# Kernel optimization log

Measured on AMD Instinct MI355X. Metric: run time of the kernel, lower is better.

The kernel has to match this reference:

```python
import jax, jax.numpy as jnp
import numpy as np

SPARSITY = 0.8  # fraction of weights zeroed (random unstructured mask)

def setup_inputs() -> dict:
    key = jax.random.key(0)
    k1, k2, k3, k4 = jax.random.split(key, 4)
    B, S, D_IN, D_OUT = 4, 2048, 4096, 4096
    x = jax.random.normal(k1, (B, S, D_IN), dtype=jnp.float32)
    weight = jax.random.normal(k2, (D_OUT, D_IN), dtype=jnp.float32) * 0.02
    bias = jax.random.normal(k3, (D_OUT,), dtype=jnp.float32) * 0.02
    # fixed binary mask: keep with prob (1 - sparsity)
    mask = (jax.random.uniform(k4, (D_OUT, D_IN)) >= SPARSITY).astype(jnp.float32)
    return {"x": x, "weight": weight, "bias": bias, "mask": mask}

def reference(x, weight, bias, mask):
    # w = weight * mask; y = x @ w.T + b   (F.linear semantics)
    w = weight * mask                      # [O, I]
    y = jnp.einsum('bsi,oi->bso', x, w)    # [B, S, O]
    return y + bias
```

## Files before the change

### kernel.cpp

```cpp
#include <hip/hip_runtime.h>
#include <hip/hip_bf16.h>
#include <stdint.h>

#define M_DIM 8192
#define N_DIM 4096
#define K_DIM 4096

#define BM 256
#define BN 256
#define BK 64
#define NT (K_DIM / BK)

typedef __attribute__((ext_vector_type(8))) __bf16 bf16x8;
typedef __attribute__((ext_vector_type(4))) float floatx4;

__device__ inline unsigned f2b(float f) {
    union { float f; unsigned u; } v; v.f = f;
    return (v.u + 0x7FFFu + ((v.u >> 16) & 1u)) >> 16;
}
__device__ inline unsigned pk2(float lo, float hi) {
    return (f2b(lo) & 0xFFFFu) | (f2b(hi) << 16);
}

__device__ inline void async_load16(const void* g, void* l) {
    __builtin_amdgcn_global_load_lds(
        (const __attribute__((address_space(1))) unsigned int*)(unsigned long long)g,
        (__attribute__((address_space(3))) unsigned int*)(unsigned int)(unsigned long long)l,
        16, 0, 0);
}

#define SFENCE() asm volatile("" ::: "memory")

#define CVT_GRID 2048
#define CVT_XBLK 1120
__global__ __launch_bounds__(256)
void cvt_all(const float4* __restrict__ x, const float4* __restrict__ w,
             const float4* __restrict__ m, uint4* __restrict__ xb,
             uint4* __restrict__ wb, int nx8, int nw8) {
    if ((int)blockIdx.x < CVT_XBLK) {
        int i = blockIdx.x * 256 + threadIdx.x;
        const int stride = CVT_XBLK * 256;
        for (; i < nx8; i += stride) {
            float4 a = x[2 * i], b = x[2 * i + 1];
            uint4 o;
            o.x = pk2(a.x, a.y); o.y = pk2(a.z, a.w);
            o.z = pk2(b.x, b.y); o.w = pk2(b.z, b.w);
            xb[i] = o;
        }
    } else {
        int i = ((int)blockIdx.x - CVT_XBLK) * 256 + threadIdx.x;
        const int stride = (CVT_GRID - CVT_XBLK) * 256;
        for (; i < nw8; i += stride) {
            float4 w0 = w[2 * i], w1 = w[2 * i + 1];
            float4 m0 = m[2 * i], m1 = m[2 * i + 1];
            uint4 o;
            o.x = pk2(w0.x * m0.x, w0.y * m0.y);
            o.y = pk2(w0.z * m0.z, w0.w * m0.w);
            o.z = pk2(w1.x * m1.x, w1.y * m1.y);
            o.w = pk2(w1.z * m1.z, w1.w * m1.w);
            wb[i] = o;
        }
    }
}

__global__ __launch_bounds__(512, 2)
void gemm_8phase(const __hip_bfloat16* __restrict__ A,
                 const __hip_bfloat16* __restrict__ B,
                 const float* __restrict__ bias,
                 float* __restrict__ C) {
    __shared__ __hip_bfloat16 As[2][2][128][64];
    __shared__ __hip_bfloat16 Bs[2][2][128][64];

    const int t    = threadIdx.x;
    const int lane = t & 63;
    const int wave = t >> 6;
    const int wm   = wave >> 2;
    const int wn   = wave & 3;
    const int lm   = lane & 15;
    const int h4   = lane >> 4;

    const int wg = (blockIdx.x & 7) * 64 + (blockIdx.x >> 3);
    const int m0 = (wg >> 4) * BM;
    const int n0 = (wg & 15) * BN;

    const int srow = t >> 3;
    const int schk = t & 7;
    const int sx   = schk ^ (srow & 7);

    const __hip_bfloat16* gA[2][2];
    const __hip_bfloat16* gB[2][2];
#pragma unroll
    for (int h = 0; h < 2; h++)
#pragma unroll
        for (int r = 0; r < 2; r++) {
            gA[h][r] = A + (size_t)(m0 + h * 128 + r * 64 + srow) * K_DIM + sx * 8;
            gB[h][r] = B + (size_t)(n0 + h * 128 + r * 64 + srow) * K_DIM + sx * 8;
        }

#define STAGE_A(b, h, r, tt) \
    async_load16(gA[h][r] + (size_t)(tt) * BK, &As[b][h][(r) * 64 + srow][schk * 8])
#define STAGE_B(b, h, r, tt) \
    async_load16(gB[h][r] + (size_t)(tt) * BK, &Bs[b][h][(r) * 64 + srow][schk * 8])

    const int cs0 = ((h4)     ^ (lm & 7)) * 8;
    const int cs1 = ((4 + h4) ^ (lm & 7)) * 8;

#define LDA(b, i, kk) \
    (*(const bf16x8*)&As[b][wm][(i) * 16 + lm][(kk) ? cs1 : cs0])
#define LDB(b, j, kk) \
    (*(const bf16x8*)&Bs[b][wn >> 1][(wn & 1) * 64 + (j) * 16 + lm][(kk) ? cs1 : cs0])

    floatx4 acc[8][4] = {};
    bf16x8 af[4][2], b01[2][2], b23[2][2];

#define MFMA16(bi, bj, B_)                                                    \
    __builtin_amdgcn_s_setprio(1);                                            \
    _Pragma("unroll") for (int i = 0; i < 4; i++)                             \
    _Pragma("unroll") for (int j = 0; j < 2; j++)                             \
    _Pragma("unroll") for (int kk = 0; kk < 2; kk++)                          \
        acc[(bi) + i][(bj) + j] = __builtin_amdgcn_mfma_f32_16x16x32_bf16(    \
            af[i][kk], B_[j][kk], acc[(bi) + i][(bj) + j], 0, 0, 0);          \
    __builtin_amdgcn_s_setprio(0);

#define KTILE(b, nb, ss)                                                      \
  { const int s_ = (ss);                                                      \
                                               \
    _Pragma("unroll") for (int i = 0; i < 4; i++) {                           \
        af[i][0] = LDA(b, i, 0); af[i][1] = LDA(b, i, 1); }                   \
    _Pragma("unroll") for (int j = 0; j < 2; j++) {                           \
        b01[j][0] = LDB(b, j, 0); b01[j][1] = LDB(b, j, 1); }                 \
    if (s_ + 1 < NT) { STAGE_A(nb, 0, 1, s_ + 1); STAGE_A(nb, 1, 1, s_ + 1); }\
    asm volatile("s_waitcnt lgkmcnt(8)" ::: "memory");                        \
    SFENCE(); __builtin_amdgcn_s_barrier();                                   \
    asm volatile("s_waitcnt lgkmcnt(0)" ::: "memory");                        \
    MFMA16(0, 0, b01)                                                         \
    SFENCE(); __builtin_amdgcn_s_barrier(); SFENCE();                         \
                                               \
    _Pragma("unroll") for (int j = 0; j < 2; j++) {                           \
        b23[j][0] = LDB(b, 2 + j, 0); b23[j][1] = LDB(b, 2 + j, 1); }         \
    if (s_ + 2 < NT) { STAGE_A(b, 0, 0, s_ + 2); STAGE_A(b, 1, 0, s_ + 2); }  \
    SFENCE(); __builtin_amdgcn_s_barrier();                                   \
    asm volatile("s_waitcnt lgkmcnt(0)" ::: "memory");                        \
    MFMA16(0, 2, b23)                                                         \
    SFENCE(); __builtin_amdgcn_s_barrier(); SFENCE();                         \
                                               \
    _Pragma("unroll") for (int i = 0; i < 4; i++) {                           \
        af[i][0] = LDA(b, 4 + i, 0); af[i][1] = LDA(b, 4 + i, 1); }           \
    if (s_ + 2 < NT) { STAGE_B(b, 0, 0, s_ + 2); STAGE_B(b, 0, 1, s_ + 2); }  \
    SFENCE(); __builtin_amdgcn_s_barrier();                                   \
    asm volatile("s_waitcnt lgkmcnt(0)" ::: "memory");                        \
    MFMA16(4, 0, b01)                                                         \
    SFENCE(); __builtin_amdgcn_s_barrier(); SFENCE();                         \
                                               \
    if (s_ + 2 < NT) { STAGE_B(b, 1, 0, s_ + 2); STAGE_B(b, 1, 1, s_ + 2); }  \
    MFMA16(4, 2, b23)                                                         \
    if (s_ + 2 < NT) asm volatile("s_waitcnt vmcnt(6)" ::: "memory");         \
    else             asm volatile("s_waitcnt vmcnt(0)" ::: "memory");         \
    SFENCE(); __builtin_amdgcn_s_barrier(); SFENCE();                         \
  }

    STAGE_A(0, 0, 0, 0); STAGE_A(0, 1, 0, 0);
    STAGE_A(0, 0, 1, 0); STAGE_A(0, 1, 1, 0);
    STAGE_B(0, 0, 0, 0); STAGE_B(0, 0, 1, 0);
    STAGE_B(0, 1, 0, 0); STAGE_B(0, 1, 1, 0);
    STAGE_A(1, 0, 0, 1); STAGE_A(1, 1, 0, 1);
    STAGE_B(1, 0, 0, 1); STAGE_B(1, 0, 1, 1);
    STAGE_B(1, 1, 0, 1); STAGE_B(1, 1, 1, 1);
    asm volatile("s_waitcnt vmcnt(6)" ::: "memory");
    __builtin_amdgcn_s_barrier();
    SFENCE();

    for (int s = 0; s < NT; s += 2) {
        KTILE(0, 1, s)
        KTILE(1, 0, s + 1)
    }

    float bv[4];
#pragma unroll
    for (int j = 0; j < 4; j++)
        bv[j] = bias[n0 + wn * 64 + j * 16 + lm];
    const int row_base = m0 + wm * 128 + h4 * 4;
    const int col_base = n0 + wn * 64 + lm;
#pragma unroll
    for (int i = 0; i < 8; i++)
#pragma unroll
        for (int j = 0; j < 4; j++) {
            const int col = col_base + j * 16;
#pragma unroll
            for (int r = 0; r < 4; r++)
                C[(size_t)(row_base + i * 16 + r) * N_DIM + col] =
                    acc[i][j][r] + bv[j];
        }
}

extern "C" void kernel_launch(void* const* d_in, const int* in_sizes, int n_in,
                              void* d_out, int out_size, void* d_ws, size_t ws_size,
                              hipStream_t stream) {
    const float* x    = (const float*)d_in[0];
    const float* w    = (const float*)d_in[1];
    const float* bias = (const float*)d_in[2];
    const float* mask = (const float*)d_in[3];
    float* out = (float*)d_out;

    __hip_bfloat16* xb = (__hip_bfloat16*)d_ws;
    __hip_bfloat16* wb = xb + (size_t)M_DIM * K_DIM;

    cvt_all<<<dim3(CVT_GRID), dim3(256), 0, stream>>>(
        (const float4*)x, (const float4*)w, (const float4*)mask,
        (uint4*)xb, (uint4*)wb, M_DIM * K_DIM / 8, N_DIM * K_DIM / 8);
    gemm_8phase<<<dim3(512), dim3(512), 0, stream>>>(xb, wb, bias, out);
}
```

Before: 527.2 us.

## Double-buffer A fragments and prefetch next tile's LDS reads across K-tiles

Splits the A-fragment registers into two sets (rows 0-3 and 4-7), so the LDS reads for the next K-tile's first phase can be issued at the end of the current tile. This lets each MFMA phase rely on barriers alone, without explicit lgkmcnt waits. Global-to-LDS staging is reordered, and the tail branches are replaced by re-staging the current tile into the same buffer. The aim is to overlap LDS reads with MFMA work and cut stall points, at the cost of more live registers and some redundant global loads on the last tiles.

```diff
diff --git a/kernel.cpp b/kernel.cpp
--- a/kernel.cpp
+++ b/kernel.cpp
@@ -111,69 +111,75 @@
     (*(const bf16x8*)&Bs[b][wn >> 1][(wn & 1) * 64 + (j) * 16 + lm][(kk) ? cs1 : cs0])
 
     floatx4 acc[8][4] = {};
-    bf16x8 af[4][2], b01[2][2], b23[2][2];
-
-#define MFMA16(bi, bj, B_)                                                    \
+    bf16x8 af03[4][2], af47[4][2], b01[2][2], b23[2][2];
+
+#define MFMA16(bi, bj, A_, B_)                                                \
     __builtin_amdgcn_s_setprio(1);                                            \
     _Pragma("unroll") for (int i = 0; i < 4; i++)                             \
     _Pragma("unroll") for (int j = 0; j < 2; j++)                             \
     _Pragma("unroll") for (int kk = 0; kk < 2; kk++)                          \
         acc[(bi) + i][(bj) + j] = __builtin_amdgcn_mfma_f32_16x16x32_bf16(    \
-            af[i][kk], B_[j][kk], acc[(bi) + i][(bj) + j], 0, 0, 0);          \
+            A_[i][kk], B_[j][kk], acc[(bi) + i][(bj) + j], 0, 0, 0);          \
     __builtin_amdgcn_s_setprio(0);
 
 #define KTILE(b, nb, ss)                                                      \
   { const int s_ = (ss);                                                      \
-                                               \
-    _Pragma("unroll") for (int i = 0; i < 4; i++) {                           \
-        af[i][0] = LDA(b, i, 0); af[i][1] = LDA(b, i, 1); }                   \
-    _Pragma("unroll") for (int j = 0; j < 2; j++) {                           \
-        b01[j][0] = LDB(b, j, 0); b01[j][1] = LDB(b, j, 1); }                 \
-    if (s_ + 1 < NT) { STAGE_A(nb, 0, 1, s_ + 1); STAGE_A(nb, 1, 1, s_ + 1); }\
-    asm volatile("s_waitcnt lgkmcnt(8)" ::: "memory");                        \
-    SFENCE(); __builtin_amdgcn_s_barrier();                                   \
-    asm volatile("s_waitcnt lgkmcnt(0)" ::: "memory");                        \
-    MFMA16(0, 0, b01)                                                         \
-    SFENCE(); __builtin_amdgcn_s_barrier(); SFENCE();                         \
-                                               \
+    const int tt = (s_ + 2 < NT) ? s_ + 2 : s_;   \
+                               \
     _Pragma("unroll") for (int j = 0; j < 2; j++) {                           \
         b23[j][0] = LDB(b, 2 + j, 0); b23[j][1] = LDB(b, 2 + j, 1); }         \
-    if (s_ + 2 < NT) { STAGE_A(b, 0, 0, s_ + 2); STAGE_A(b, 1, 0, s_ + 2); }  \
-    SFENCE(); __builtin_amdgcn_s_barrier();                                   \
-    asm volatile("s_waitcnt lgkmcnt(0)" ::: "memory");                        \
-    MFMA16(0, 2, b23)                                                         \
-    SFENCE(); __builtin_amdgcn_s_barrier(); SFENCE();                         \
-                                               \
+    SFENCE(); __builtin_amdgcn_s_barrier();                                   \
+    MFMA16(0, 0, af03, b01)                                                   \
+    SFENCE(); __builtin_amdgcn_s_barrier();                                   \
+            \
     _Pragma("unroll") for (int i = 0; i < 4; i++) {                           \
-        af[i][0] = LDA(b, 4 + i, 0); af[i][1] = LDA(b, 4 + i, 1); }           \
-    if (s_ + 2 < NT) { STAGE_B(b, 0, 0, s_ + 2); STAGE_B(b, 0, 1, s_ + 2); }  \
-    SFENCE(); __builtin_amdgcn_s_barrier();                                   \
-    asm volatile("s_waitcnt lgkmcnt(0)" ::: "memory");                        \
-    MFMA16(4, 0, b01)                                                         \
-    SFENCE(); __builtin_amdgcn_s_barrier(); SFENCE();                         \
-                                               \
-    if (s_ + 2 < NT) { STAGE_B(b, 1, 0, s_ + 2); STAGE_B(b, 1, 1, s_ + 2); }  \
-    MFMA16(4, 2, b23)                                                         \
-    if (s_ + 2 < NT) asm volatile("s_waitcnt vmcnt(6)" ::: "memory");         \
-    else             asm volatile("s_waitcnt vmcnt(0)" ::: "memory");         \
-    SFENCE(); __builtin_amdgcn_s_barrier(); SFENCE();                         \
+        af47[i][0] = LDA(b, 4 + i, 0); af47[i][1] = LDA(b, 4 + i, 1); }       \
+    STAGE_A(b, 0, 0, tt); STAGE_A(b, 1, 0, tt);                               \
+    SFENCE(); __builtin_amdgcn_s_barrier();                                   \
+    MFMA16(0, 2, af03, b23)                                                   \
+    SFENCE(); __builtin_amdgcn_s_barrier();                                   \
+                             \
+    STAGE_B(b, 0, 0, tt); STAGE_B(b, 0, 1, tt);                               \
+    STAGE_B(b, 1, 0, tt); STAGE_B(b, 1, 1, tt);                               \
+    SFENCE(); __builtin_amdgcn_s_barrier();                                   \
+    MFMA16(4, 0, af47, b01)                                                   \
+    SFENCE(); __builtin_amdgcn_s_barrier();                                   \
+    \
+    asm volatile("s_waitcnt vmcnt(6)" ::: "memory");                          \
+    if (s_ + 1 < NT) {                                                        \
+        _Pragma("unroll") for (int i = 0; i < 4; i++) {                       \
+            af03[i][0] = LDA(nb, i, 0); af03[i][1] = LDA(nb, i, 1); }         \
+        _Pragma("unroll") for (int j = 0; j < 2; j++) {                       \
+            b01[j][0] = LDB(nb, j, 0); b01[j][1] = LDB(nb, j, 1); }           \
+    }                                                                         \
+    STAGE_A(b, 0, 1, tt); STAGE_A(b, 1, 1, tt);                               \
+    SFENCE(); __builtin_amdgcn_s_barrier();                                   \
+    MFMA16(4, 2, af47, b23)                                                   \
+    SFENCE(); __builtin_amdgcn_s_barrier();                                   \
   }
 
     STAGE_A(0, 0, 0, 0); STAGE_A(0, 1, 0, 0);
-    STAGE_A(0, 0, 1, 0); STAGE_A(0, 1, 1, 0);
     STAGE_B(0, 0, 0, 0); STAGE_B(0, 0, 1, 0);
     STAGE_B(0, 1, 0, 0); STAGE_B(0, 1, 1, 0);
+    STAGE_A(0, 0, 1, 0); STAGE_A(0, 1, 1, 0);
     STAGE_A(1, 0, 0, 1); STAGE_A(1, 1, 0, 1);
     STAGE_B(1, 0, 0, 1); STAGE_B(1, 0, 1, 1);
     STAGE_B(1, 1, 0, 1); STAGE_B(1, 1, 1, 1);
-    asm volatile("s_waitcnt vmcnt(6)" ::: "memory");
+    STAGE_A(1, 0, 1, 1); STAGE_A(1, 1, 1, 1);
+    asm volatile("s_waitcnt vmcnt(8)" ::: "memory");
     __builtin_amdgcn_s_barrier();
+    SFENCE();
+#pragma unroll
+    for (int i = 0; i < 4; i++) { af03[i][0] = LDA(0, i, 0); af03[i][1] = LDA(0, i, 1); }
+#pragma unroll
+    for (int j = 0; j < 2; j++) { b01[j][0] = LDB(0, j, 0); b01[j][1] = LDB(0, j, 1); }
     SFENCE();
 
     for (int s = 0; s < NT; s += 2) {
         KTILE(0, 1, s)
         KTILE(1, 0, s + 1)
     }
+    asm volatile("s_waitcnt vmcnt(0)" ::: "memory");
 
     float bv[4];
 #pragma unroll
```

New measurement: 532.9 us. No clear change (+1.1%).
